# Kernel tuning notes

Hardware: AMD Instinct MI355X
Metric: run time of the kernel (lower is better)

## Reference

```python
import jax, jax.numpy as jnp
import numpy as np

NQ = 64
BIG = 1e10

FILTERS = np.array([[1,0,0,1,0,0,1,0,0],
                    [0,0,0,0,0,0,1,1,1],
                    [0,0,1,0,0,1,0,0,1],
                    [1,1,1,0,0,0,0,0,0],
                    [0,0,0,1,0,0,1,1,0],
                    [0,0,0,0,0,1,0,1,1],
                    [0,1,1,0,0,1,0,0,0],
                    [1,1,0,1,0,0,0,0,0]], dtype=np.float32).reshape(8,1,3,3)


def _conv2d(x, k):
    return jax.lax.conv_general_dilated(x, k, (1,1), 'SAME',
                                        dimension_numbers=('NCHW','OIHW','NCHW'))


def _maxpool3(x):  # 3x3 stride-1 maxpool, pad=1 (pads with -inf like torch)
    return jax.lax.reduce_window(x, -jnp.inf, jax.lax.max, (1,1,3,3), (1,1,1,1), 'SAME')


def setup_inputs() -> dict:
    key = jax.random.key(0)
    ks = jax.random.split(key, 5)
    b, h, w = 2, 240, 320
    n = 2 * h * w  # 153600 points
    fx = fy = 300.0
    cx, cy = w / 2.0, h / 2.0
    z  = jax.random.uniform(ks[0], (b, n), minval=1.0, maxval=10.0)
    u  = jax.random.uniform(ks[1], (b, n), minval=0.0, maxval=float(w))
    v  = jax.random.uniform(ks[2], (b, n), minval=0.0, maxval=float(h))
    xw = (u - cx) / fx * z
    yw = (v - cy) / fy * z
    rgb = jax.random.uniform(ks[3], (b, 3, n))
    pp = jnp.concatenate([xw[:, None], yw[:, None], z[:, None],
                          jnp.ones((b, 1, n), jnp.float32), rgb], axis=1)  # [b,7,n]
    conf = jax.random.uniform(ks[4], (b, n))
    pose_w2c = jnp.tile(jnp.eye(4, dtype=jnp.float32)[None], (b, 1, 1))
    K = jnp.tile(jnp.array([[fx, 0, cx], [0, fy, cy], [0, 0, 1.0]], jnp.float32)[None], (b, 1, 1))
    filters = jnp.asarray(FILTERS)
    return {"pp": pp, "conf": conf, "pose_w2c": pose_w2c, "K": K,
            "filters": filters, "h": h, "w": w}


def reference(pp, conf, pose_w2c, K, filters, h, w,
              znear=0.1, zfar=1000.0, conf_thresh=0.0):
    b, _, n = pp.shape
    # world -> camera (wsz=1 so the hi-res pool is identity)
    pc = jnp.einsum('bij,bjn->bin', pose_w2c, pp[:, :4])          # [b,4,n]
    z  = jnp.abs(pc[:, 2])                                        # [b,n]
    xc = pc[:, 0] * K[:, 0, 0][:, None] / z + K[:, 0, 2][:, None]
    yc = pc[:, 1] * K[:, 1, 1][:, None] / z + K[:, 1, 2][:, None]
    x = jnp.round(xc).astype(jnp.int32)
    y = jnp.round(yc).astype(jnp.int32)
    oob = ((x < 0) | (x >= w) | (y < 0) | (y >= h) |
           (z < znear) | (z > zfar) | (conf <= conf_thresh))
    # inverse-depth quantization bounds over valid points only
    inv_lo = 1.0 / jnp.where(oob, 1e-10, z)   # oob -> 1e10, drops out of min
    inv_hi = 1.0 / jnp.where(oob, BIG, z)     # oob -> 1e-10, drops out of max
    dmin = jnp.min(inv_lo, axis=-1, keepdims=True)
    dmax = jnp.max(inv_hi, axis=-1, keepdims=True)
    do = ((inv_hi - dmin) / (dmax - dmin) * (NQ - 1)).astype(jnp.int32)  # [b,n]

    # scatter points into [b, NQ, h, w] z-buffer bins (drop invalid)
    size = b * NQ * h * w
    bidx = jnp.arange(b, dtype=jnp.int32)[:, None]
    idx = ((bidx * NQ + do) * h + y) * w + x
    idx = jnp.where(oob, size, idx).reshape(-1)   # 'size' is out of bounds -> dropped
    zf = z.astype(jnp.float32).reshape(-1)
    dmap = jnp.zeros((size,), jnp.float32).at[idx].set(zf, mode='drop').reshape(b, NQ, h, w)
    cmap = jnp.full((size,), -1.0, jnp.float32).at[idx].set(conf.reshape(-1), mode='drop').reshape(b, NQ, h, w)
    rgb_pts = pp[:, 4:].transpose(0, 2, 1).reshape(-1, 3).astype(jnp.float32)
    rgb = jnp.zeros((size, 3), jnp.float32).at[idx].set(rgb_pts, mode='drop').reshape(b, NQ, h, w, 3)

    # z-buffer composite: nearest non-empty bin per pixel
    dmap = jnp.where(dmap <= 0, BIG, dmap)
    min_idx = jnp.argmin(dmap, axis=1)                             # [b,h,w]
    dflat = jnp.min(dmap, axis=1)
    dflat = jnp.where(dflat >= BIG, 0.0, dflat)
    cflat = jnp.take_along_axis(cmap, min_idx[:, None], axis=1)[:, 0]
    cflat = jnp.maximum(cflat, 0.0)                                # cmap_[cmap_<0]=0
    rflat = jnp.take_along_axis(rgb, min_idx[:, None, :, :, None], axis=1)[:, 0]  # [b,h,w,3]

    # vertical flip (torch.flip over h)
    depths = dflat[:, ::-1][:, None]                               # [b,1,h,w]
    confs  = cflat[:, ::-1][:, None]
    rgbs   = jnp.transpose(rflat[:, ::-1], (0, 3, 1, 2))           # [b,3,h,w]

    # hole filling: 2 iterations of oriented-filter tests + 3x3 max pooling
    ones_k = jnp.ones((1, 1, 3, 3), jnp.float32)
    for _ in range(2):
        tofill = (_conv2d(depths, ones_k) > 0) & (depths <= 0)
        o = _conv2d(depths, filters)                               # [b,8,h,w]
        fill = (jnp.abs(jnp.prod(o, axis=1, keepdims=True)) > 1e-10) & tofill
        f = fill.astype(jnp.float32)
        depths = depths * (1 - f) + f * _maxpool3(depths)
        confs  = confs  * (1 - f) + f * _maxpool3(confs)
        rgbs   = rgbs   * (1 - f) + f * _maxpool3(rgbs)
    return depths, confs, rgbs
```

## Files before the change

kernel.cpp:

```cpp
#include <hip/hip_runtime.h>
#include <stdint.h>

#define NQ 64
#define ZNEAR 0.1f
#define ZFAR 1000.0f
#define FT 16

__device__ __forceinline__ float wave_min_f(float v) {
    #pragma unroll
    for (int off = 1; off < 64; off <<= 1)
        v = fminf(v, __shfl_xor(v, off, 64));
    return v;
}
__device__ __forceinline__ float wave_max_f(float v) {
    #pragma unroll
    for (int off = 1; off < 64; off <<= 1)
        v = fmaxf(v, __shfl_xor(v, off, 64));
    return v;
}

__global__ void k_project(const float* __restrict__ pp, const float* __restrict__ conf,
                          const float* __restrict__ pose, const float* __restrict__ Km,
                          const int* __restrict__ hp, const int* __restrict__ wp,
                          int B, int n,
                          float* __restrict__ zbuf, unsigned* __restrict__ packed,
                          float4* __restrict__ cr4,
                          float* __restrict__ pmin, float* __restrict__ pmax, int nBlk,
                          unsigned* __restrict__ pixwin, int pixTot) {
    int bb = blockIdx.y;
    int i = blockIdx.x * blockDim.x + threadIdx.x;
    size_t ztid = ((size_t)blockIdx.y * gridDim.x + blockIdx.x) * blockDim.x + threadIdx.x;
    if (ztid < (size_t)pixTot) pixwin[ztid] = 0u;

    int h = *hp, w = *wp;
    float inv_lo = INFINITY;
    float inv_hi = 0.0f;
    if (i < n) {
        const float* P  = pose + (size_t)bb * 16;
        const float* km = Km   + (size_t)bb * 9;
        const float* pb = pp   + (size_t)bb * 7 * n;
        float X  = pb[0 * (size_t)n + i];
        float Y  = pb[1 * (size_t)n + i];
        float Z  = pb[2 * (size_t)n + i];
        float Wc = pb[3 * (size_t)n + i];
        float pc0 = P[0] * X + P[1] * Y + P[2]  * Z + P[3]  * Wc;
        float pc1 = P[4] * X + P[5] * Y + P[6]  * Z + P[7]  * Wc;
        float pc2 = P[8] * X + P[9] * Y + P[10] * Z + P[11] * Wc;
        float z = fabsf(pc2);
        float xc = pc0 * km[0] / z + km[2];
        float yc = pc1 * km[4] / z + km[5];
        float xr = rintf(xc);
        float yr = rintf(yc);
        float cf = conf[(size_t)bb * n + i];
        bool valid = (xr >= 0.0f) && (xr <= (float)(w - 1)) &&
                     (yr >= 0.0f) && (yr <= (float)(h - 1)) &&
                     (z >= ZNEAR) && (z <= ZFAR) && (cf > 0.0f);
        unsigned px = valid ? (unsigned)(int)xr : 0u;
        unsigned py = valid ? (unsigned)(int)yr : 0u;
        size_t p = (size_t)bb * n + i;
        zbuf[p] = z;
        packed[p] = (valid ? 0x80000000u : 0u) | px | (py << 12);
        cr4[p] = make_float4(cf, pb[4 * (size_t)n + i], pb[5 * (size_t)n + i], pb[6 * (size_t)n + i]);
        inv_lo = valid ? (1.0f / z) : (1.0f / 1e-10f);
        inv_hi = valid ? (1.0f / z) : (1.0f / 1e10f);
    }
    __shared__ float smin[4], smax[4];
    float wmin = wave_min_f(inv_lo);
    float wmax = wave_max_f(inv_hi);
    int lane = threadIdx.x & 63, wid = threadIdx.x >> 6;
    if (lane == 0) { smin[wid] = wmin; smax[wid] = wmax; }
    __syncthreads();
    if (threadIdx.x == 0) {
        pmin[(size_t)bb * nBlk + blockIdx.x] = fminf(fminf(smin[0], smin[1]), fminf(smin[2], smin[3]));
        pmax[(size_t)bb * nBlk + blockIdx.x] = fmaxf(fmaxf(smax[0], smax[1]), fmaxf(smax[2], smax[3]));
    }
}

__global__ void k_scatter(const float* __restrict__ zbuf, const unsigned* __restrict__ packed,
                          const float* __restrict__ pminb, const float* __restrict__ pmaxb, int nBlk,
                          const int* __restrict__ hp, const int* __restrict__ wp,
                          int B, int n, unsigned* __restrict__ pixwin) {
    __shared__ float smin[4], smax[4];
    __shared__ float sdlo[8], sdhi[8];
    for (int bb = 0; bb < B; ++bb) {
        float lmin = INFINITY, lmax = 0.0f;
        for (int k = threadIdx.x; k < nBlk; k += blockDim.x) {
            lmin = fminf(lmin, pminb[(size_t)bb * nBlk + k]);
            lmax = fmaxf(lmax, pmaxb[(size_t)bb * nBlk + k]);
        }
        lmin = wave_min_f(lmin);
        lmax = wave_max_f(lmax);
        int lane = threadIdx.x & 63, wid = threadIdx.x >> 6;
        if (lane == 0) { smin[wid] = lmin; smax[wid] = lmax; }
        __syncthreads();
        if (threadIdx.x == 0) {
            sdlo[bb] = fminf(fminf(smin[0], smin[1]), fminf(smin[2], smin[3]));
            sdhi[bb] = fmaxf(fmaxf(smax[0], smax[1]), fmaxf(smax[2], smax[3]));
        }
        __syncthreads();
    }
    int p = blockIdx.x * blockDim.x + threadIdx.x;
    if (p >= B * n) return;
    unsigned pk = packed[p];
    if (!(pk & 0x80000000u)) return;
    int bb = p / n;
    int i = p - bb * n;
    float inv = 1.0f / zbuf[p];
    float dlo = sdlo[bb], dhi = sdhi[bb];
    int dq = (int)((inv - dlo) / (dhi - dlo) * (float)(NQ - 1));
    int h = *hp, w = *wp;
    int x = (int)(pk & 0xFFFu);
    int y = (int)((pk >> 12) & 0xFFFu);
    unsigned key = ((unsigned)dq << 20) | (unsigned)(i + 1);
    atomicMax(&pixwin[(size_t)bb * h * w + (size_t)y * w + x], key);
}

__global__ void k_resfill(const float* __restrict__ zbuf, const float4* __restrict__ cr4,
                          const unsigned* __restrict__ pixwin,
                          const float* __restrict__ filt,
                          const int* __restrict__ hp, const int* __restrict__ wp,
                          int B, int n, float* __restrict__ out, int pixTot) {
    int h = *hp, w = *wp;
    int tilesX = (w + FT - 1) / FT;
    int tilesY = (h + FT - 1) / FT;
    int tile = blockIdx.x;
    if (tile >= tilesX * tilesY) return;
    int bb = blockIdx.y;
    int tY = tile / tilesX, tX = tile - tY * tilesX;
    int gy0 = tY * FT - 2, gx0 = tX * FT - 2;
    int hw = h * w;

    __shared__ float s_f[72];
    __shared__ float s_in[5][20][20];
    __shared__ float s_m[5][18][18];
    int tid = threadIdx.x;
    if (tid < 72) s_f[tid] = filt[tid];

    for (int idx = tid; idx < 400; idx += blockDim.x) {
        int yy = idx / 20, xx = idx - yy * 20;
        int gy = gy0 + yy, gx = gx0 + xx;
        float v0 = 0.0f, v1 = 0.0f, v2 = 0.0f, v3 = 0.0f, v4 = 0.0f;
        if (((unsigned)gy < (unsigned)h) && ((unsigned)gx < (unsigned)w)) {
            int ys = h - 1 - gy;
            unsigned key = pixwin[(size_t)bb * hw + (size_t)ys * w + gx];
            if (key) {
                int i = (int)(key & 0xFFFFFu) - 1;
                size_t p = (size_t)bb * n + i;
                v0 = zbuf[p];
                float4 cr = cr4[p];
                v1 = cr.x; v2 = cr.y; v3 = cr.z; v4 = cr.w;
            }
        }
        s_in[0][yy][xx] = v0;
        s_in[1][yy][xx] = v1;
        s_in[2][yy][xx] = v2;
        s_in[3][yy][xx] = v3;
        s_in[4][yy][xx] = v4;
    }
    __syncthreads();

    for (int idx = tid; idx < 324; idx += blockDim.x) {
        int py = idx / 18, px = idx - py * 18;
        int sy = py + 1, sx = px + 1;
        int gy = gy0 + sy, gx = gx0 + sx;
        bool vc = ((unsigned)gy < (unsigned)h) && ((unsigned)gx < (unsigned)w);
        float d[9];
        #pragma unroll
        for (int t = 0; t < 9; ++t) d[t] = s_in[0][sy + t / 3 - 1][sx + t % 3 - 1];
        float s = 0.0f;
        #pragma unroll
        for (int t = 0; t < 9; ++t) s += d[t];
        float dc0 = d[4];
        float ov[5];
        #pragma unroll
        for (int ch = 0; ch < 5; ++ch) ov[ch] = s_in[ch][sy][sx];
        if ((s > 0.0f) && (dc0 <= 0.0f)) {
            float prod = 1.0f;
            #pragma unroll
            for (int k = 0; k < 8; ++k) {
                float o = 0.0f;
                #pragma unroll
                for (int t = 0; t < 9; ++t) o += s_f[k * 9 + t] * d[t];
                prod *= o;
            }
            if (fabsf(prod) > 1e-10f) {
                #pragma unroll
                for (int ch = 0; ch < 5; ++ch) {
                    float m = -INFINITY;
                    #pragma unroll
                    for (int t = 0; t < 9; ++t) {
                        int ny = gy + t / 3 - 1, nx = gx + t % 3 - 1;
                        if (((unsigned)ny < (unsigned)h) && ((unsigned)nx < (unsigned)w))
                            m = fmaxf(m, s_in[ch][sy + t / 3 - 1][sx + t % 3 - 1]);
                    }
                    ov[ch] = m;
                }
            }
        }
        if (!vc) { ov[0] = 0.0f; ov[1] = 0.0f; ov[2] = 0.0f; ov[3] = 0.0f; ov[4] = 0.0f; }
        #pragma unroll
        for (int ch = 0; ch < 5; ++ch) s_m[ch][py][px] = ov[ch];
    }
    __syncthreads();

    int ly = tid >> 4, lx = tid & 15;
    int gy = tY * FT + ly, gx = tX * FT + lx;
    if (((unsigned)gy < (unsigned)h) && ((unsigned)gx < (unsigned)w)) {
        int sy = ly + 1, sx = lx + 1;
        float d[9];
        #pragma unroll
        for (int t = 0; t < 9; ++t) d[t] = s_m[0][sy + t / 3 - 1][sx + t % 3 - 1];
        float s = 0.0f;
        #pragma unroll
        for (int t = 0; t < 9; ++t) s += d[t];
        float dc0 = d[4];
        float ov[5];
        #pragma unroll
        for (int ch = 0; ch < 5; ++ch) ov[ch] = s_m[ch][sy][sx];
        if ((s > 0.0f) && (dc0 <= 0.0f)) {
            float prod = 1.0f;
            #pragma unroll
            for (int k = 0; k < 8; ++k) {
                float o = 0.0f;
                #pragma unroll
                for (int t = 0; t < 9; ++t) o += s_f[k * 9 + t] * d[t];
                prod *= o;
            }
            if (fabsf(prod) > 1e-10f) {
                #pragma unroll
                for (int ch = 0; ch < 5; ++ch) {
                    float m = -INFINITY;
                    #pragma unroll
                    for (int t = 0; t < 9; ++t) {
                        int ny = gy + t / 3 - 1, nx = gx + t % 3 - 1;
                        if (((unsigned)ny < (unsigned)h) && ((unsigned)nx < (unsigned)w))
                            m = fmaxf(m, s_m[ch][sy + t / 3 - 1][sx + t % 3 - 1]);
                    }
                    ov[ch] = m;
                }
            }
        }
        size_t g = (size_t)gy * w + gx;
        out[(size_t)bb * hw + g] = ov[0];
        out[(size_t)pixTot + (size_t)bb * hw + g] = ov[1];
        size_t rb = 2 * (size_t)pixTot;
        out[rb + (((size_t)bb * 3 + 0) * hw) + g] = ov[2];
        out[rb + (((size_t)bb * 3 + 1) * hw) + g] = ov[3];
        out[rb + (((size_t)bb * 3 + 2) * hw) + g] = ov[4];
    }
}

static inline size_t align16(size_t x) { return (x + 15) & ~(size_t)15; }

extern "C" void kernel_launch(void* const* d_in, const int* in_sizes, int n_in,
                              void* d_out, int out_size, void* d_ws, size_t ws_size,
                              hipStream_t stream) {
    const float* pp   = (const float*)d_in[0];
    const float* conf = (const float*)d_in[1];
    const float* pose = (const float*)d_in[2];
    const float* Km   = (const float*)d_in[3];
    const float* filt = (const float*)d_in[4];
    const int*   hp   = (const int*)d_in[5];
    const int*   wp   = (const int*)d_in[6];

    int B = in_sizes[2] / 16;
    int n = in_sizes[1] / B;
    size_t pix = (size_t)out_size / 5;
    size_t npts = (size_t)B * n;
    size_t hw = pix / B;

    const int bs = 256;
    int nBlk = (n + bs - 1) / bs;

    char* ws = (char*)d_ws;
    size_t off = 0;
    unsigned* pixwin = (unsigned*)(ws + off);  off = align16(off + pix * 4);
    float* zbuf   = (float*)(ws + off);        off = align16(off + npts * 4);
    unsigned* packed = (unsigned*)(ws + off);  off = align16(off + npts * 4);
    float4* cr4   = (float4*)(ws + off);       off = align16(off + npts * 16);
    float* pminb  = (float*)(ws + off);        off = align16(off + (size_t)B * nBlk * 4);
    float* pmaxb  = (float*)(ws + off);        off = align16(off + (size_t)B * nBlk * 4);

    float* out = (float*)d_out;
    int pixI = (int)pix;

    dim3 gproj(nBlk, B);
    k_project<<<gproj, bs, 0, stream>>>(pp, conf, pose, Km, hp, wp, B, n,
                                        zbuf, packed, cr4, pminb, pmaxb, nBlk,
                                        pixwin, pixI);

    int nptsI = (int)npts;
    k_scatter<<<(nptsI + bs - 1) / bs, bs, 0, stream>>>(zbuf, packed, pminb, pmaxb, nBlk,
                                                        hp, wp, B, n, pixwin);

    size_t tileBound = hw / (FT * FT) + hw / FT + 2;
    dim3 gfill((unsigned)tileBound, B);
    k_resfill<<<gfill, bs, 0, stream>>>(zbuf, cr4, pixwin, filt, hp, wp, B, n, out, pixI);
}
```

Before: 104.7 us.

## Scatter payload via 64-bit keyed atomicMax per channel, drop cr4 staging

Instead of resolving the z-buffer winner to a point index and gathering its attributes later, the scatter kernel now issues five 64-bit atomicMax ops per point, each packing the depth-priority key in the high word and a channel value in the low word. This removes the cr4 staging buffer and the dependent indirect gathers in the fill kernel. The fill kernel becomes a persistent grid of 1024 blocks looping over tiles, and the per-pixel zeroing is vectorised to uint4 with a grid-stride loop. In exchange it does five times as many atomics on 64-bit words and zeroes and reads a larger pixel buffer.

```diff
diff --git a/kernel.cpp b/kernel.cpp
--- a/kernel.cpp
+++ b/kernel.cpp
@@ -24,13 +24,14 @@
                           const int* __restrict__ hp, const int* __restrict__ wp,
                           int B, int n,
                           float* __restrict__ zbuf, unsigned* __restrict__ packed,
-                          float4* __restrict__ cr4,
                           float* __restrict__ pmin, float* __restrict__ pmax, int nBlk,
-                          unsigned* __restrict__ pixwin, int pixTot) {
+                          uint4* __restrict__ pixz16, size_t nZero16) {
     int bb = blockIdx.y;
     int i = blockIdx.x * blockDim.x + threadIdx.x;
     size_t ztid = ((size_t)blockIdx.y * gridDim.x + blockIdx.x) * blockDim.x + threadIdx.x;
-    if (ztid < (size_t)pixTot) pixwin[ztid] = 0u;
+    size_t zstr = (size_t)gridDim.x * gridDim.y * blockDim.x;
+    uint4 zz = make_uint4(0u, 0u, 0u, 0u);
+    for (size_t k = ztid; k < nZero16; k += zstr) pixz16[k] = zz;
 
     int h = *hp, w = *wp;
     float inv_lo = INFINITY;
@@ -60,7 +61,6 @@
         size_t p = (size_t)bb * n + i;
         zbuf[p] = z;
         packed[p] = (valid ? 0x80000000u : 0u) | px | (py << 12);
-        cr4[p] = make_float4(cf, pb[4 * (size_t)n + i], pb[5 * (size_t)n + i], pb[6 * (size_t)n + i]);
         inv_lo = valid ? (1.0f / z) : (1.0f / 1e-10f);
         inv_hi = valid ? (1.0f / z) : (1.0f / 1e10f);
     }
@@ -76,10 +76,11 @@
     }
 }
 
-__global__ void k_scatter(const float* __restrict__ zbuf, const unsigned* __restrict__ packed,
+__global__ void k_scatter(const float* __restrict__ pp, const float* __restrict__ conf,
+                          const float* __restrict__ zbuf, const unsigned* __restrict__ packed,
                           const float* __restrict__ pminb, const float* __restrict__ pmaxb, int nBlk,
                           const int* __restrict__ hp, const int* __restrict__ wp,
-                          int B, int n, unsigned* __restrict__ pixwin) {
+                          int B, int n, unsigned long long* __restrict__ pixw, int pixTot) {
     __shared__ float smin[4], smax[4];
     __shared__ float sdlo[8], sdhi[8];
     for (int bb = 0; bb < B; ++bb) {
@@ -105,148 +106,153 @@
     if (!(pk & 0x80000000u)) return;
     int bb = p / n;
     int i = p - bb * n;
-    float inv = 1.0f / zbuf[p];
+    float z = zbuf[p];
+    float inv = 1.0f / z;
     float dlo = sdlo[bb], dhi = sdhi[bb];
     int dq = (int)((inv - dlo) / (dhi - dlo) * (float)(NQ - 1));
     int h = *hp, w = *wp;
     int x = (int)(pk & 0xFFFu);
     int y = (int)((pk >> 12) & 0xFFFu);
     unsigned key = ((unsigned)dq << 20) | (unsigned)(i + 1);
-    atomicMax(&pixwin[(size_t)bb * h * w + (size_t)y * w + x], key);
-}
-
-__global__ void k_resfill(const float* __restrict__ zbuf, const float4* __restrict__ cr4,
-                          const unsigned* __restrict__ pixwin,
-                          const float* __restrict__ filt,
-                          const int* __restrict__ hp, const int* __restrict__ wp,
-                          int B, int n, float* __restrict__ out, int pixTot) {
+    unsigned long long hi = (unsigned long long)key << 32;
+    size_t pxi = (size_t)bb * h * w + (size_t)y * w + x;
+    const float* pb = pp + (size_t)bb * 7 * n;
+    atomicMax(&pixw[pxi],                     hi | (unsigned long long)__float_as_uint(z));
+    atomicMax(&pixw[(size_t)pixTot     + pxi], hi | (unsigned long long)__float_as_uint(conf[(size_t)bb * n + i]));
+    atomicMax(&pixw[2 * (size_t)pixTot + pxi], hi | (unsigned long long)__float_as_uint(pb[4 * (size_t)n + i]));
+    atomicMax(&pixw[3 * (size_t)pixTot + pxi], hi | (unsigned long long)__float_as_uint(pb[5 * (size_t)n + i]));
+    atomicMax(&pixw[4 * (size_t)pixTot + pxi], hi | (unsigned long long)__float_as_uint(pb[6 * (size_t)n + i]));
+}
+
+__global__ void __launch_bounds__(256, 4)
+k_resfill(const unsigned long long* __restrict__ pixw,
+          const float* __restrict__ filt,
+          const int* __restrict__ hp, const int* __restrict__ wp,
+          int B, float* __restrict__ out, int pixTot) {
     int h = *hp, w = *wp;
     int tilesX = (w + FT - 1) / FT;
     int tilesY = (h + FT - 1) / FT;
-    int tile = blockIdx.x;
-    if (tile >= tilesX * tilesY) return;
-    int bb = blockIdx.y;
-    int tY = tile / tilesX, tX = tile - tY * tilesX;
-    int gy0 = tY * FT - 2, gx0 = tX * FT - 2;
+    int TPB = tilesX * tilesY;
+    int T = TPB * B;
     int hw = h * w;
+    int tid = threadIdx.x;
 
     __shared__ float s_f[72];
     __shared__ float s_in[5][20][20];
     __shared__ float s_m[5][18][18];
-    int tid = threadIdx.x;
     if (tid < 72) s_f[tid] = filt[tid];
 
-    for (int idx = tid; idx < 400; idx += blockDim.x) {
-        int yy = idx / 20, xx = idx - yy * 20;
-        int gy = gy0 + yy, gx = gx0 + xx;
-        float v0 = 0.0f, v1 = 0.0f, v2 = 0.0f, v3 = 0.0f, v4 = 0.0f;
-        if (((unsigned)gy < (unsigned)h) && ((unsigned)gx < (unsigned)w)) {
-            int ys = h - 1 - gy;
-            unsigned key = pixwin[(size_t)bb * hw + (size_t)ys * w + gx];
-            if (key) {
-                int i = (int)(key & 0xFFFFFu) - 1;
-                size_t p = (size_t)bb * n + i;
-                v0 = zbuf[p];
-                float4 cr = cr4[p];
-                v1 = cr.x; v2 = cr.y; v3 = cr.z; v4 = cr.w;
+    for (int t = blockIdx.x; t < T; t += gridDim.x) {
+        int bb = t / TPB;
+        int tile = t - bb * TPB;
+        int tY = tile / tilesX, tX = tile - tY * tilesX;
+        int gy0 = tY * FT - 2, gx0 = tX * FT - 2;
+
+        for (int idx = tid; idx < 400; idx += blockDim.x) {
+            int yy = idx / 20, xx = idx - yy * 20;
+            int gy = gy0 + yy, gx = gx0 + xx;
+            float v[5] = {0.0f, 0.0f, 0.0f, 0.0f, 0.0f};
+            if (((unsigned)gy < (unsigned)h) && ((unsigned)gx < (unsigned)w)) {
+                int ys = h - 1 - gy;
+                size_t g = (size_t)bb * hw + (size_t)ys * w + gx;
+                #pragma unroll
+                for (int ch = 0; ch < 5; ++ch)
+                    v[ch] = __uint_as_float((unsigned)(pixw[(size_t)ch * pixTot + g] & 0xFFFFFFFFull));
             }
-        }
-        s_in[0][yy][xx] = v0;
-        s_in[1][yy][xx] = v1;
-        s_in[2][yy][xx] = v2;
-        s_in[3][yy][xx] = v3;
-        s_in[4][yy][xx] = v4;
-    }
-    __syncthreads();
-
-    for (int idx = tid; idx < 324; idx += blockDim.x) {
-        int py = idx / 18, px = idx - py * 18;
-        int sy = py + 1, sx = px + 1;
-        int gy = gy0 + sy, gx = gx0 + sx;
-        bool vc = ((unsigned)gy < (unsigned)h) && ((unsigned)gx < (unsigned)w);
-        float d[9];
-        #pragma unroll
-        for (int t = 0; t < 9; ++t) d[t] = s_in[0][sy + t / 3 - 1][sx + t % 3 - 1];
-        float s = 0.0f;
-        #pragma unroll
-        for (int t = 0; t < 9; ++t) s += d[t];
-        float dc0 = d[4];
-        float ov[5];
-        #pragma unroll
-        for (int ch = 0; ch < 5; ++ch) ov[ch] = s_in[ch][sy][sx];
-        if ((s > 0.0f) && (dc0 <= 0.0f)) {
-            float prod = 1.0f;
-            #pragma unroll
-            for (int k = 0; k < 8; ++k) {
-                float o = 0.0f;
+            #pragma unroll
+            for (int ch = 0; ch < 5; ++ch) s_in[ch][yy][xx] = v[ch];
+        }
+        __syncthreads();
+
+        for (int idx = tid; idx < 324; idx += blockDim.x) {
+            int py = idx / 18, px = idx - py * 18;
+            int sy = py + 1, sx = px + 1;
+            int gy = gy0 + sy, gx = gx0 + sx;
+            bool vc = ((unsigned)gy < (unsigned)h) && ((unsigned)gx < (unsigned)w);
+            float d[9];
+            #pragma unroll
+            for (int t9 = 0; t9 < 9; ++t9) d[t9] = s_in[0][sy + t9 / 3 - 1][sx + t9 % 3 - 1];
+            float s = 0.0f;
+            #pragma unroll
+            for (int t9 = 0; t9 < 9; ++t9) s += d[t9];
+            float dc0 = d[4];
+            float ov[5];
+            #pragma unroll
+            for (int ch = 0; ch < 5; ++ch) ov[ch] = s_in[ch][sy][sx];
+            if ((s > 0.0f) && (dc0 <= 0.0f)) {
+                float prod = 1.0f;
                 #pragma unroll
-                for (int t = 0; t < 9; ++t) o += s_f[k * 9 + t] * d[t];
-                prod *= o;
-            }
-            if (fabsf(prod) > 1e-10f) {
-                #pragma unroll
-                for (int ch = 0; ch < 5; ++ch) {
-                    float m = -INFINITY;
+                for (int k = 0; k < 8; ++k) {
+                    float o = 0.0f;
                     #pragma unroll
-                    for (int t = 0; t < 9; ++t) {
-                        int ny = gy + t / 3 - 1, nx = gx + t % 3 - 1;
-                        if (((unsigned)ny < (unsigned)h) && ((unsigned)nx < (unsigned)w))
-                            m = fmaxf(m, s_in[ch][sy + t / 3 - 1][sx + t % 3 - 1]);
+                    for (int t9 = 0; t9 < 9; ++t9) o += s_f[k * 9 + t9] * d[t9];
+                    prod *= o;
+                }
+                if (fabsf(prod) > 1e-10f) {
+                    #pragma unroll
+                    for (int ch = 0; ch < 5; ++ch) {
+                        float m = -INFINITY;
+                        #pragma unroll
+                        for (int t9 = 0; t9 < 9; ++t9) {
+                            int ny = gy + t9 / 3 - 1, nx = gx + t9 % 3 - 1;
+                            if (((unsigned)ny < (unsigned)h) && ((unsigned)nx < (unsigned)w))
+                                m = fmaxf(m, s_in[ch][sy + t9 / 3 - 1][sx + t9 % 3 - 1]);
+                        }
+                        ov[ch] = m;
                     }
-                    ov[ch] = m;
                 }
             }
-        }
-        if (!vc) { ov[0] = 0.0f; ov[1] = 0.0f; ov[2] = 0.0f; ov[3] = 0.0f; ov[4] = 0.0f; }
-        #pragma unroll
-        for (int ch = 0; ch < 5; ++ch) s_m[ch][py][px] = ov[ch];
-    }
-    __syncthreads();
-
-    int ly = tid >> 4, lx = tid & 15;
-    int gy = tY * FT + ly, gx = tX * FT + lx;
-    if (((unsigned)gy < (unsigned)h) && ((unsigned)gx < (unsigned)w)) {
-        int sy = ly + 1, sx = lx + 1;
-        float d[9];
-        #pragma unroll
-        for (int t = 0; t < 9; ++t) d[t] = s_m[0][sy + t / 3 - 1][sx + t % 3 - 1];
-        float s = 0.0f;
-        #pragma unroll
-        for (int t = 0; t < 9; ++t) s += d[t];
-        float dc0 = d[4];
-        float ov[5];
-        #pragma unroll
-        for (int ch = 0; ch < 5; ++ch) ov[ch] = s_m[ch][sy][sx];
-        if ((s > 0.0f) && (dc0 <= 0.0f)) {
-            float prod = 1.0f;
-            #pragma unroll
-            for (int k = 0; k < 8; ++k) {
-                float o = 0.0f;
+            if (!vc) { ov[0] = 0.0f; ov[1] = 0.0f; ov[2] = 0.0f; ov[3] = 0.0f; ov[4] = 0.0f; }
+            #pragma unroll
+            for (int ch = 0; ch < 5; ++ch) s_m[ch][py][px] = ov[ch];
+        }
+        __syncthreads();
+
+        int ly = tid >> 4, lx = tid & 15;
+        int gy = tY * FT + ly, gx = tX * FT + lx;
+        if (((unsigned)gy < (unsigned)h) && ((unsigned)gx < (unsigned)w)) {
+            int sy = ly + 1, sx = lx + 1;
+            float d[9];
+            #pragma unroll
+            for (int t9 = 0; t9 < 9; ++t9) d[t9] = s_m[0][sy + t9 / 3 - 1][sx + t9 % 3 - 1];
+            float s = 0.0f;
+            #pragma unroll
+            for (int t9 = 0; t9 < 9; ++t9) s += d[t9];
+            float dc0 = d[4];
+            float ov[5];
+            #pragma unroll
+            for (int ch = 0; ch < 5; ++ch) ov[ch] = s_m[ch][sy][sx];
+            if ((s > 0.0f) && (dc0 <= 0.0f)) {
+                float prod = 1.0f;
                 #pragma unroll
-                for (int t = 0; t < 9; ++t) o += s_f[k * 9 + t] * d[t];
-                prod *= o;
-            }
-            if (fabsf(prod) > 1e-10f) {
-                #pragma unroll
-                for (int ch = 0; ch < 5; ++ch) {
-                    float m = -INFINITY;
+                for (int k = 0; k < 8; ++k) {
+                    float o = 0.0f;
                     #pragma unroll
-                    for (int t = 0; t < 9; ++t) {
-                        int ny = gy + t / 3 - 1, nx = gx + t % 3 - 1;
-                        if (((unsigned)ny < (unsigned)h) && ((unsigned)nx < (unsigned)w))
-                            m = fmaxf(m, s_m[ch][sy + t / 3 - 1][sx + t % 3 - 1]);
+                    for (int t9 = 0; t9 < 9; ++t9) o += s_f[k * 9 + t9] * d[t9];
+                    prod *= o;
+                }
+                if (fabsf(prod) > 1e-10f) {
+                    #pragma unroll
+                    for (int ch = 0; ch < 5; ++ch) {
+                        float m = -INFINITY;
+                        #pragma unroll
+                        for (int t9 = 0; t9 < 9; ++t9) {
+                            int ny = gy + t9 / 3 - 1, nx = gx + t9 % 3 - 1;
+                            if (((unsigned)ny < (unsigned)h) && ((unsigned)nx < (unsigned)w))
+                                m = fmaxf(m, s_m[ch][sy + t9 / 3 - 1][sx + t9 % 3 - 1]);
+                        }
+                        ov[ch] = m;
                     }
-                    ov[ch] = m;
                 }
             }
-        }
-        size_t g = (size_t)gy * w + gx;
-        out[(size_t)bb * hw + g] = ov[0];
-        out[(size_t)pixTot + (size_t)bb * hw + g] = ov[1];
-        size_t rb = 2 * (size_t)pixTot;
-        out[rb + (((size_t)bb * 3 + 0) * hw) + g] = ov[2];
-        out[rb + (((size_t)bb * 3 + 1) * hw) + g] = ov[3];
-        out[rb + (((size_t)bb * 3 + 2) * hw) + g] = ov[4];
+            size_t g = (size_t)gy * w + gx;
+            out[(size_t)bb * hw + g] = ov[0];
+            out[(size_t)pixTot + (size_t)bb * hw + g] = ov[1];
+            size_t rb = 2 * (size_t)pixTot;
+            out[rb + (((size_t)bb * 3 + 0) * hw) + g] = ov[2];
+            out[rb + (((size_t)bb * 3 + 1) * hw) + g] = ov[3];
+            out[rb + (((size_t)bb * 3 + 2) * hw) + g] = ov[4];
+        }
     }
 }
 
@@ -267,33 +273,31 @@
     int n = in_sizes[1] / B;
     size_t pix = (size_t)out_size / 5;
     size_t npts = (size_t)B * n;
-    size_t hw = pix / B;
 
     const int bs = 256;
     int nBlk = (n + bs - 1) / bs;
 
     char* ws = (char*)d_ws;
     size_t off = 0;
-    unsigned* pixwin = (unsigned*)(ws + off);  off = align16(off + pix * 4);
+    unsigned long long* pixw = (unsigned long long*)(ws + off);  off = align16(off + 5 * pix * 8);
     float* zbuf   = (float*)(ws + off);        off = align16(off + npts * 4);
     unsigned* packed = (unsigned*)(ws + off);  off = align16(off + npts * 4);
-    float4* cr4   = (float4*)(ws + off);       off = align16(off + npts * 16);
     float* pminb  = (float*)(ws + off);        off = align16(off + (size_t)B * nBlk * 4);
     float* pmaxb  = (float*)(ws + off);        off = align16(off + (size_t)B * nBlk * 4);
 
     float* out = (float*)d_out;
     int pixI = (int)pix;
+    size_t nZero16 = 5 * pix * 8 / 16;
 
     dim3 gproj(nBlk, B);
     k_project<<<gproj, bs, 0, stream>>>(pp, conf, pose, Km, hp, wp, B, n,
-                                        zbuf, packed, cr4, pminb, pmaxb, nBlk,
-                                        pixwin, pixI);
+                                        zbuf, packed, pminb, pmaxb, nBlk,
+                                        (uint4*)pixw, nZero16);
 
     int nptsI = (int)npts;
-    k_scatter<<<(nptsI + bs - 1) / bs, bs, 0, stream>>>(zbuf, packed, pminb, pmaxb, nBlk,
-                                                        hp, wp, B, n, pixwin);
-
-    size_t tileBound = hw / (FT * FT) + hw / FT + 2;
-    dim3 gfill((unsigned)tileBound, B);
-    k_resfill<<<gfill, bs, 0, stream>>>(zbuf, cr4, pixwin, filt, hp, wp, B, n, out, pixI);
-}
+    k_scatter<<<(nptsI + bs - 1) / bs, bs, 0, stream>>>(pp, conf, zbuf, packed,
+                                                        pminb, pmaxb, nBlk,
+                                                        hp, wp, B, n, pixw, pixI);
+
+    k_resfill<<<1024, bs, 0, stream>>>(pixw, filt, hp, wp, B, out, pixI);
+}
```

Result: slower. 148.9 us (+42.2%).

## Interleave depth with conf/rgb records and make hole-fill kernel grid-stride persistent

Applied to the files above, without the earlier changes.

The projection kernel now writes depth, confidence and RGB into one 32-byte record per point. The fill kernel can then fetch a winning point's attributes with two adjacent float4 loads instead of separate gathers from two arrays. The fill kernel becomes a grid-stride loop over (batch, tile) with a fixed 1024-block grid and launch bounds. The cost is a larger per-point workspace write in the projection pass, including padding.

```diff
diff --git a/kernel.cpp b/kernel.cpp
--- a/kernel.cpp
+++ b/kernel.cpp
@@ -24,7 +24,7 @@
                           const int* __restrict__ hp, const int* __restrict__ wp,
                           int B, int n,
                           float* __restrict__ zbuf, unsigned* __restrict__ packed,
-                          float4* __restrict__ cr4,
+                          float4* __restrict__ zcr8,
                           float* __restrict__ pmin, float* __restrict__ pmax, int nBlk,
                           unsigned* __restrict__ pixwin, int pixTot) {
     int bb = blockIdx.y;
@@ -60,7 +60,8 @@
         size_t p = (size_t)bb * n + i;
         zbuf[p] = z;
         packed[p] = (valid ? 0x80000000u : 0u) | px | (py << 12);
-        cr4[p] = make_float4(cf, pb[4 * (size_t)n + i], pb[5 * (size_t)n + i], pb[6 * (size_t)n + i]);
+        zcr8[2 * p]     = make_float4(z, cf, pb[4 * (size_t)n + i], pb[5 * (size_t)n + i]);
+        zcr8[2 * p + 1] = make_float4(pb[6 * (size_t)n + i], 0.0f, 0.0f, 0.0f);
         inv_lo = valid ? (1.0f / z) : (1.0f / 1e-10f);
         inv_hi = valid ? (1.0f / z) : (1.0f / 1e10f);
     }
@@ -115,142 +116,146 @@
     atomicMax(&pixwin[(size_t)bb * h * w + (size_t)y * w + x], key);
 }
 
-__global__ void k_resfill(const float* __restrict__ zbuf, const float4* __restrict__ cr4,
-                          const unsigned* __restrict__ pixwin,
-                          const float* __restrict__ filt,
-                          const int* __restrict__ hp, const int* __restrict__ wp,
-                          int B, int n, float* __restrict__ out, int pixTot) {
+__global__ void __launch_bounds__(256, 4)
+k_resfill(const float4* __restrict__ zcr8, const unsigned* __restrict__ pixwin,
+          const float* __restrict__ filt,
+          const int* __restrict__ hp, const int* __restrict__ wp,
+          int B, int n, float* __restrict__ out, int pixTot) {
     int h = *hp, w = *wp;
     int tilesX = (w + FT - 1) / FT;
     int tilesY = (h + FT - 1) / FT;
-    int tile = blockIdx.x;
-    if (tile >= tilesX * tilesY) return;
-    int bb = blockIdx.y;
-    int tY = tile / tilesX, tX = tile - tY * tilesX;
-    int gy0 = tY * FT - 2, gx0 = tX * FT - 2;
+    int TPB = tilesX * tilesY;
+    int T = TPB * B;
     int hw = h * w;
+    int tid = threadIdx.x;
 
     __shared__ float s_f[72];
     __shared__ float s_in[5][20][20];
     __shared__ float s_m[5][18][18];
-    int tid = threadIdx.x;
     if (tid < 72) s_f[tid] = filt[tid];
 
-    for (int idx = tid; idx < 400; idx += blockDim.x) {
-        int yy = idx / 20, xx = idx - yy * 20;
-        int gy = gy0 + yy, gx = gx0 + xx;
-        float v0 = 0.0f, v1 = 0.0f, v2 = 0.0f, v3 = 0.0f, v4 = 0.0f;
+    for (int t = blockIdx.x; t < T; t += gridDim.x) {
+        int bb = t / TPB;
+        int tile = t - bb * TPB;
+        int tY = tile / tilesX, tX = tile - tY * tilesX;
+        int gy0 = tY * FT - 2, gx0 = tX * FT - 2;
+
+        for (int idx = tid; idx < 400; idx += blockDim.x) {
+            int yy = idx / 20, xx = idx - yy * 20;
+            int gy = gy0 + yy, gx = gx0 + xx;
+            float v0 = 0.0f, v1 = 0.0f, v2 = 0.0f, v3 = 0.0f, v4 = 0.0f;
+            if (((unsigned)gy < (unsigned)h) && ((unsigned)gx < (unsigned)w)) {
+                int ys = h - 1 - gy;
+                unsigned key = pixwin[(size_t)bb * hw + (size_t)ys * w + gx];
+                if (key) {
+                    int i = (int)(key & 0xFFFFFu) - 1;
+                    size_t p = (size_t)bb * n + i;
+                    float4 a = zcr8[2 * p];
+                    float4 c = zcr8[2 * p + 1];
+                    v0 = a.x; v1 = a.y; v2 = a.z; v3 = a.w; v4 = c.x;
+                }
+            }
+            s_in[0][yy][xx] = v0;
+            s_in[1][yy][xx] = v1;
+            s_in[2][yy][xx] = v2;
+            s_in[3][yy][xx] = v3;
+            s_in[4][yy][xx] = v4;
+        }
+        __syncthreads();
+
+        for (int idx = tid; idx < 324; idx += blockDim.x) {
+            int py = idx / 18, px = idx - py * 18;
+            int sy = py + 1, sx = px + 1;
+            int gy = gy0 + sy, gx = gx0 + sx;
+            bool vc = ((unsigned)gy < (unsigned)h) && ((unsigned)gx < (unsigned)w);
+            float d[9];
+            #pragma unroll
+            for (int t9 = 0; t9 < 9; ++t9) d[t9] = s_in[0][sy + t9 / 3 - 1][sx + t9 % 3 - 1];
+            float s = 0.0f;
+            #pragma unroll
+            for (int t9 = 0; t9 < 9; ++t9) s += d[t9];
+            float dc0 = d[4];
+            float ov[5];
+            #pragma unroll
+            for (int ch = 0; ch < 5; ++ch) ov[ch] = s_in[ch][sy][sx];
+            if ((s > 0.0f) && (dc0 <= 0.0f)) {
+                float prod = 1.0f;
+                #pragma unroll
+                for (int k = 0; k < 8; ++k) {
+                    float o = 0.0f;
+                    #pragma unroll
+                    for (int t9 = 0; t9 < 9; ++t9) o += s_f[k * 9 + t9] * d[t9];
+                    prod *= o;
+                }
+                if (fabsf(prod) > 1e-10f) {
+                    #pragma unroll
+                    for (int ch = 0; ch < 5; ++ch) {
+                        float m = -INFINITY;
+                        #pragma unroll
+                        for (int t9 = 0; t9 < 9; ++t9) {
+                            int ny = gy + t9 / 3 - 1, nx = gx + t9 % 3 - 1;
+                            if (((unsigned)ny < (unsigned)h) && ((unsigned)nx < (unsigned)w))
+                                m = fmaxf(m, s_in[ch][sy + t9 / 3 - 1][sx + t9 % 3 - 1]);
+                        }
+                        ov[ch] = m;
+                    }
+                }
+            }
+            if (!vc) { ov[0] = 0.0f; ov[1] = 0.0f; ov[2] = 0.0f; ov[3] = 0.0f; ov[4] = 0.0f; }
+            #pragma unroll
+            for (int ch = 0; ch < 5; ++ch) s_m[ch][py][px] = ov[ch];
+        }
+        __syncthreads();
+
+        int ly = tid >> 4, lx = tid & 15;
+        int gy = tY * FT + ly, gx = tX * FT + lx;
         if (((unsigned)gy < (unsigned)h) && ((unsigned)gx < (unsigned)w)) {
-            int ys = h - 1 - gy;
-            unsigned key = pixwin[(size_t)bb * hw + (size_t)ys * w + gx];
-            if (key) {
-                int i = (int)(key & 0xFFFFFu) - 1;
-                size_t p = (size_t)bb * n + i;
-                v0 = zbuf[p];
-                float4 cr = cr4[p];
-                v1 = cr.x; v2 = cr.y; v3 = cr.z; v4 = cr.w;
+            int sy = ly + 1, sx = lx + 1;
+            float d[9];
+            #pragma unroll
+            for (int t9 = 0; t9 < 9; ++t9) d[t9] = s_m[0][sy + t9 / 3 - 1][sx + t9 % 3 - 1];
+            float s = 0.0f;
+            #pragma unroll
+            for (int t9 = 0; t9 < 9; ++t9) s += d[t9];
+            float dc0 = d[4];
+            float ov[5];
+            #pragma unroll
+            for (int ch = 0; ch < 5; ++ch) ov[ch] = s_m[ch][sy][sx];
+            if ((s > 0.0f) && (dc0 <= 0.0f)) {
+                float prod = 1.0f;
+                #pragma unroll
+                for (int k = 0; k < 8; ++k) {
+                    float o = 0.0f;
+                    #pragma unroll
+                    for (int t9 = 0; t9 < 9; ++t9) o += s_f[k * 9 + t9] * d[t9];
+                    prod *= o;
+                }
+                if (fabsf(prod) > 1e-10f) {
+                    #pragma unroll
+                    for (int ch = 0; ch < 5; ++ch) {
+                        float m = -INFINITY;
+                        #pragma unroll
+                        for (int t9 = 0; t9 < 9; ++t9) {
+                            int ny = gy + t9 / 3 - 1, nx = gx + t9 % 3 - 1;
+                            if (((unsigned)ny < (unsigned)h) && ((unsigned)nx < (unsigned)w))
+                                m = fmaxf(m, s_m[ch][sy + t9 / 3 - 1][sx + t9 % 3 - 1]);
+                        }
+                        ov[ch] = m;
+                    }
+                }
             }
-        }
-        s_in[0][yy][xx] = v0;
-        s_in[1][yy][xx] = v1;
-        s_in[2][yy][xx] = v2;
-        s_in[3][yy][xx] = v3;
-        s_in[4][yy][xx] = v4;
+            size_t g = (size_t)gy * w + gx;
+            out[(size_t)bb * hw + g] = ov[0];
+            out[(size_t)pixTot + (size_t)bb * hw + g] = ov[1];
+            size_t rb = 2 * (size_t)pixTot;
+            out[rb + (((size_t)bb * 3 + 0) * hw) + g] = ov[2];
+            out[rb + (((size_t)bb * 3 + 1) * hw) + g] = ov[3];
+            out[rb + (((size_t)bb * 3 + 2) * hw) + g] = ov[4];
+        }
     }
-    __syncthreads();
-
-    for (int idx = tid; idx < 324; idx += blockDim.x) {
-        int py = idx / 18, px = idx - py * 18;
-        int sy = py + 1, sx = px + 1;
-        int gy = gy0 + sy, gx = gx0 + sx;
-        bool vc = ((unsigned)gy < (unsigned)h) && ((unsigned)gx < (unsigned)w);
-        float d[9];
-        #pragma unroll
-        for (int t = 0; t < 9; ++t) d[t] = s_in[0][sy + t / 3 - 1][sx + t % 3 - 1];
-        float s = 0.0f;
-        #pragma unroll
-        for (int t = 0; t < 9; ++t) s += d[t];
-        float dc0 = d[4];
-        float ov[5];
-        #pragma unroll
-        for (int ch = 0; ch < 5; ++ch) ov[ch] = s_in[ch][sy][sx];
-        if ((s > 0.0f) && (dc0 <= 0.0f)) {
-            float prod = 1.0f;
-            #pragma unroll
-            for (int k = 0; k < 8; ++k) {
-                float o = 0.0f;
-                #pragma unroll
-                for (int t = 0; t < 9; ++t) o += s_f[k * 9 + t] * d[t];
-                prod *= o;
-            }
-            if (fabsf(prod) > 1e-10f) {
-                #pragma unroll
-                for (int ch = 0; ch < 5; ++ch) {
-                    float m = -INFINITY;
-                    #pragma unroll
-                    for (int t = 0; t < 9; ++t) {
-                        int ny = gy + t / 3 - 1, nx = gx + t % 3 - 1;
-                        if (((unsigned)ny < (unsigned)h) && ((unsigned)nx < (unsigned)w))
-                            m = fmaxf(m, s_in[ch][sy + t / 3 - 1][sx + t % 3 - 1]);
-                    }
-                    ov[ch] = m;
-                }
-            }
-        }
-        if (!vc) { ov[0] = 0.0f; ov[1] = 0.0f; ov[2] = 0.0f; ov[3] = 0.0f; ov[4] = 0.0f; }
-        #pragma unroll
-        for (int ch = 0; ch < 5; ++ch) s_m[ch][py][px] = ov[ch];
-    }
-    __syncthreads();
-
-    int ly = tid >> 4, lx = tid & 15;
-    int gy = tY * FT + ly, gx = tX * FT + lx;
-    if (((unsigned)gy < (unsigned)h) && ((unsigned)gx < (unsigned)w)) {
-        int sy = ly + 1, sx = lx + 1;
-        float d[9];
-        #pragma unroll
-        for (int t = 0; t < 9; ++t) d[t] = s_m[0][sy + t / 3 - 1][sx + t % 3 - 1];
-        float s = 0.0f;
-        #pragma unroll
-        for (int t = 0; t < 9; ++t) s += d[t];
-        float dc0 = d[4];
-        float ov[5];
-        #pragma unroll
-        for (int ch = 0; ch < 5; ++ch) ov[ch] = s_m[ch][sy][sx];
-        if ((s > 0.0f) && (dc0 <= 0.0f)) {
-            float prod = 1.0f;
-            #pragma unroll
-            for (int k = 0; k < 8; ++k) {
-                float o = 0.0f;
-                #pragma unroll
-                for (int t = 0; t < 9; ++t) o += s_f[k * 9 + t] * d[t];
-                prod *= o;
-            }
-            if (fabsf(prod) > 1e-10f) {
-                #pragma unroll
-                for (int ch = 0; ch < 5; ++ch) {
-                    float m = -INFINITY;
-                    #pragma unroll
-                    for (int t = 0; t < 9; ++t) {
-                        int ny = gy + t / 3 - 1, nx = gx + t % 3 - 1;
-                        if (((unsigned)ny < (unsigned)h) && ((unsigned)nx < (unsigned)w))
-                            m = fmaxf(m, s_m[ch][sy + t / 3 - 1][sx + t % 3 - 1]);
-                    }
-                    ov[ch] = m;
-                }
-            }
-        }
-        size_t g = (size_t)gy * w + gx;
-        out[(size_t)bb * hw + g] = ov[0];
-        out[(size_t)pixTot + (size_t)bb * hw + g] = ov[1];
-        size_t rb = 2 * (size_t)pixTot;
-        out[rb + (((size_t)bb * 3 + 0) * hw) + g] = ov[2];
-        out[rb + (((size_t)bb * 3 + 1) * hw) + g] = ov[3];
-        out[rb + (((size_t)bb * 3 + 2) * hw) + g] = ov[4];
-    }
-}
-
-static inline size_t align16(size_t x) { return (x + 15) & ~(size_t)15; }
+}
+
+static inline size_t align32(size_t x) { return (x + 31) & ~(size_t)31; }
 
 extern "C" void kernel_launch(void* const* d_in, const int* in_sizes, int n_in,
                               void* d_out, int out_size, void* d_ws, size_t ws_size,
@@ -267,33 +272,30 @@
     int n = in_sizes[1] / B;
     size_t pix = (size_t)out_size / 5;
     size_t npts = (size_t)B * n;
-    size_t hw = pix / B;
 
     const int bs = 256;
     int nBlk = (n + bs - 1) / bs;
 
     char* ws = (char*)d_ws;
     size_t off = 0;
-    unsigned* pixwin = (unsigned*)(ws + off);  off = align16(off + pix * 4);
-    float* zbuf   = (float*)(ws + off);        off = align16(off + npts * 4);
-    unsigned* packed = (unsigned*)(ws + off);  off = align16(off + npts * 4);
-    float4* cr4   = (float4*)(ws + off);       off = align16(off + npts * 16);
-    float* pminb  = (float*)(ws + off);        off = align16(off + (size_t)B * nBlk * 4);
-    float* pmaxb  = (float*)(ws + off);        off = align16(off + (size_t)B * nBlk * 4);
+    unsigned* pixwin = (unsigned*)(ws + off); off = align32(off + pix * 4);
+    float4* zcr8  = (float4*)(ws + off);      off = align32(off + npts * 32);
+    float* zbuf   = (float*)(ws + off);       off = align32(off + npts * 4);
+    unsigned* packed = (unsigned*)(ws + off); off = align32(off + npts * 4);
+    float* pminb  = (float*)(ws + off);       off = align32(off + (size_t)B * nBlk * 4);
+    float* pmaxb  = (float*)(ws + off);       off = align32(off + (size_t)B * nBlk * 4);
 
     float* out = (float*)d_out;
     int pixI = (int)pix;
 
     dim3 gproj(nBlk, B);
     k_project<<<gproj, bs, 0, stream>>>(pp, conf, pose, Km, hp, wp, B, n,
-                                        zbuf, packed, cr4, pminb, pmaxb, nBlk,
+                                        zbuf, packed, zcr8, pminb, pmaxb, nBlk,
                                         pixwin, pixI);
 
     int nptsI = (int)npts;
     k_scatter<<<(nptsI + bs - 1) / bs, bs, 0, stream>>>(zbuf, packed, pminb, pmaxb, nBlk,
                                                         hp, wp, B, n, pixwin);
 
-    size_t tileBound = hw / (FT * FT) + hw / FT + 2;
-    dim3 gfill((unsigned)tileBound, B);
-    k_resfill<<<gfill, bs, 0, stream>>>(zbuf, cr4, pixwin, filt, hp, wp, B, n, out, pixI);
-}
+    k_resfill<<<1024, bs, 0, stream>>>(zcr8, pixwin, filt, hp, wp, B, n, out, pixI);
+}
```

Measured after the change: 105.4 us (median of 2 runs). No clear change (+0.7%).
